# Performance work log

Hardware: AMD Instinct MI355X
Metric: run time of the kernel (lower is better)

Reference implementation:

```python
import jax, jax.numpy as jnp
import numpy as np
from jax import lax

B, N, D, H, K = 4096, 25, 256, 8, 3  # batch*frames, nodes, d_model, heads, conv kernel


def _layernorm(x, g, b, eps=1e-5):
    mu = jnp.mean(x, axis=-1, keepdims=True)
    var = jnp.var(x, axis=-1, keepdims=True)
    return (x - mu) * lax.rsqrt(var + eps) * g + b


def _conv1d(x_bdn, w):
    # x_bdn: [B, D, N], w: [D_out, D_in, K], padding=K//2 (same as torch Conv1d)
    return lax.conv_general_dilated(x_bdn, w, window_strides=(1,),
                                    padding=[(K // 2, K // 2)],
                                    dimension_numbers=('NCH', 'OIH', 'NCH'))


def setup_inputs() -> dict:
    key = jax.random.key(0)
    ks = jax.random.split(key, 12)
    x = jax.random.normal(ks[0], (B, N, D), dtype=jnp.float32)
    # symmetric adjacency with self-loops (skeleton graph surrogate)
    a = jax.random.bernoulli(ks[1], 0.3, (N, N))
    adj = a | a.T | jnp.eye(N, dtype=bool)
    cs = 1.0 / np.sqrt(D * K)
    wq = jax.random.normal(ks[2], (D, D, K), dtype=jnp.float32) * cs
    wk = jax.random.normal(ks[3], (D, D, K), dtype=jnp.float32) * cs
    wv = jax.random.normal(ks[4], (D, D, K), dtype=jnp.float32) * cs
    gq = jnp.ones((D,), jnp.float32); bq = jnp.zeros((D,), jnp.float32)
    gk = jnp.ones((D,), jnp.float32); bk = jnp.zeros((D,), jnp.float32)
    gv = jnp.ones((D,), jnp.float32); bv = jnp.zeros((D,), jnp.float32)
    rel_table = jax.random.normal(ks[5], (2 * N - 1, H), dtype=jnp.float32) * 0.02
    local_bias = jnp.zeros((H, N, N), jnp.float32)
    wo = jax.random.normal(ks[6], (D, D), dtype=jnp.float32) * (1.0 / np.sqrt(D))
    bo = jnp.zeros((D,), jnp.float32)
    return dict(x=x, adj=adj, wq=wq, wk=wk, wv=wv, gq=gq, bq=bq, gk=gk, bk=bk,
                gv=gv, bv=bv, rel_table=rel_table, local_bias=local_bias, wo=wo, bo=bo)


def reference(x, adj, wq, wk, wv, gq, bq, gk, bk, gv, bv, rel_table, local_bias, wo, bo):
    b, n, d = x.shape
    h = local_bias.shape[0]
    dk = d // h
    xp = x.transpose(0, 2, 1)  # [B, D, N]
    # conv QKV projection over node axis + per-projection LayerNorm + residual
    q = x + _layernorm(_conv1d(xp, wq).transpose(0, 2, 1), gq, bq)
    k = x + _layernorm(_conv1d(xp, wk).transpose(0, 2, 1), gk, bk)
    v = x + _layernorm(_conv1d(xp, wv).transpose(0, 2, 1), gv, bv)
    qh = q.reshape(b, n, h, dk).transpose(0, 2, 1, 3)  # [B, H, N, dk]
    kh = k.reshape(b, n, h, dk).transpose(0, 2, 1, 3)
    vh = v.reshape(b, n, h, dk).transpose(0, 2, 1, 3)
    scores = jnp.einsum('bhnd,bhmd->bhnm', qh, kh) / np.sqrt(dk)
    # relative positional bias over node indices
    coords = jnp.arange(n)
    idx = coords[:, None] - coords[None, :] + n - 1  # [N, N]
    rel = rel_table[idx].transpose(2, 0, 1)  # [H, N, N]
    scores = scores + rel[None] + local_bias[None]
    # adjacency mask (local attention): non-neighbors -> -inf
    scores = jnp.where(adj[None, None], scores, jnp.finfo(scores.dtype).min)
    attn = jax.nn.softmax(scores, axis=-1)
    out = jnp.einsum('bhnm,bhmd->bhnd', attn, vh)  # [B, H, N, dk]
    out = out.transpose(0, 2, 1, 3).reshape(b, n, d)
    return out @ wo.T + bo
```

## Files before the change

kernel.cpp:

```cpp
#include <hip/hip_runtime.h>

#define BB 4096
#define NN 25
#define DD 256
#define HH 8
#define DKH 32
#define MM (BB*NN)

typedef __bf16 bf16;
typedef bf16 bf16x8 __attribute__((ext_vector_type(8)));
typedef bf16 bf16x4 __attribute__((ext_vector_type(4)));
typedef float f32x4 __attribute__((ext_vector_type(4)));
typedef float f32x16 __attribute__((ext_vector_type(16)));
typedef int   i32x4 __attribute__((ext_vector_type(4)));
typedef _Float16 h16;
typedef h16 h16x2 __attribute__((ext_vector_type(2)));
typedef h16 h16x4 __attribute__((ext_vector_type(4)));
typedef h16 h16x8 __attribute__((ext_vector_type(8)));

__device__ __forceinline__ void async_load16(const void* g, void* l) {
  __builtin_amdgcn_global_load_lds(
      (const __attribute__((address_space(1))) unsigned int*)g,
      (__attribute__((address_space(3))) unsigned int*)l, 16, 0, 0);
}

#define SCHED_FENCE() __builtin_amdgcn_sched_barrier(0)
#define BARRIER() do { SCHED_FENCE(); __builtin_amdgcn_s_barrier(); SCHED_FENCE(); } while (0)

__global__ __launch_bounds__(256) void k_prep(
    const float* __restrict__ x, bf16* __restrict__ xpad,
    const float* __restrict__ wq, const float* __restrict__ wk, const float* __restrict__ wv,
    const float* __restrict__ rel, const float* __restrict__ lb, const float* __restrict__ wo,
    const void* __restrict__ adj_raw,
    bf16* __restrict__ Wt, h16* __restrict__ woF, float* __restrict__ mbF2) {
  if (blockIdx.x < 13824) {
    int idx = (blockIdx.x * 256 + threadIdx.x) * 8;
    const int total = BB * 27 * 256;
    if (idx >= total) return;
    int b = idx / (27 * 256);
    int rem = idx - b * 27 * 256;
    int j = rem >> 8;
    int d = rem & 255;
    bf16x8 o;
    if (j >= 1 && j <= 25) {
      const float* src = x + ((b * 25 + (j - 1)) * 256 + d);
      #pragma unroll
      for (int t = 0; t < 8; ++t) o[t] = (bf16)src[t];
    } else {
      #pragma unroll
      for (int t = 0; t < 8; ++t) o[t] = (bf16)0.0f;
    }
    *(bf16x8*)(xpad + idx) = o;
    return;
  }
  const int NWT = 768 * 768;
  const int NMB = HH * 64 * 16;
  const int NWF = 8 * 16 * 64 * 8;
  const int total = NWT + NMB + NWF;
  for (int i = (blockIdx.x - 13824) * 256 + threadIdx.x; i < total; i += 512 * 256) {
    if (i < NWT) {
      int j = i / 768, kk = i - j * 768;
      int proj = j >> 8, jo = j & 255;
      int tap = kk >> 8, di = kk & 255;
      const float* w = (proj == 0) ? wq : ((proj == 1) ? wk : wv);
      Wt[i] = (bf16)w[(jo * 256 + di) * 3 + tap];
    } else if (i < NWT + NMB) {
      int t = i - NWT;
      int h = t >> 10;
      int L = (t >> 4) & 63;
      int r = t & 15;
      int iq = L & 31;
      int m = (r & 3) + 8 * (r >> 2) + 4 * (L >> 5);
      float v;
      if (m >= 25) {
        v = -1e30f;
      } else if (iq >= 25) {
        v = 0.0f;
      } else {
        const unsigned char* bytes = (const unsigned char*)adj_raw;
        bool u8 = false;
        for (int s = 0; s < 625; ++s) {
          if ((s & 3) && bytes[s]) { u8 = true; break; }
        }
        int amask = u8 ? (bytes[iq * 25 + m] ? 1 : 0)
                       : (((const int*)adj_raw)[iq * 25 + m] ? 1 : 0);
        v = amask ? (rel[(iq - m + 24) * HH + h] + lb[h * 625 + iq * 25 + m]) : -1e30f;
      }
      mbF2[t] = v;
    } else {
      int e = i - NWT - NMB;
      int c = e & 7, ln = (e >> 3) & 63, nt = (e >> 9) & 15, ks = e >> 13;
      int col = nt * 16 + (ln & 15);
      int k = ks * 32 + (ln >> 4) * 8 + c;
      woF[e] = (h16)wo[col * 256 + k];
    }
  }
}

__global__ __launch_bounds__(512, 2) void k_qkv_gemm8(const bf16* __restrict__ xpad,
                                                      const bf16* __restrict__ Wt,
                                                      bf16* __restrict__ conv) {
  __shared__ bf16 Ab[2][256 * 64];
  __shared__ bf16 Bb[2][256 * 64];

  const int L = blockIdx.x;
  const int sw = (L & 7) * 150 + (L >> 3);
  const int n0 = (sw % 3) * 256;
  const int m0 = (sw / 3) * 256;

  const int tid = threadIdx.x;
  const int lane = tid & 63, wave = tid >> 6;
  const int t16 = lane & 15, quad = lane >> 4;
  const int wr = wave >> 2, wc = wave & 3;

  const int srow = tid >> 3;
  const int sc = ((tid & 7) << 4) ^ ((srow & 7) << 4);
  int aOff[4], bOff[4];
  #pragma unroll
  for (int q = 0; q < 4; ++q) {
    int row = q * 64 + srow;
    int gm = m0 + row;
    int b = gm / 25;
    int n = gm - b * 25;
    aOff[q] = (b * 27 + n) * 512 + sc;
    bOff[q] = (n0 + row) * 1536 + sc;
  }

  const int axr = (t16 & 7) << 3;
  int aoffs[2], boffs[2];
  #pragma unroll
  for (int kk = 0; kk < 2; ++kk) {
    aoffs[kk] = (wr * 128 + t16) * 64 + ((kk * 32 + quad * 8) ^ axr);
    boffs[kk] = (wc * 64 + t16) * 64 + ((kk * 32 + quad * 8) ^ axr);
  }

  f32x4 acc[8][4];
  #pragma unroll
  for (int i = 0; i < 8; ++i)
    #pragma unroll
    for (int j = 0; j < 4; ++j) acc[i][j] = (f32x4){0.f, 0.f, 0.f, 0.f};

  #define ST_B(bufi, tt) do {                                              \
    char* lb_ = (char*)&Bb[bufi][0] + wave * 1024;                         \
    _Pragma("unroll")                                                      \
    for (int q_ = 0; q_ < 4; ++q_)                                         \
      async_load16((const char*)Wt + bOff[q_] + (tt) * 128, lb_ + q_ * 8192); \
  } while (0)
  #define ST_A(bufi, tt) do {                                              \
    char* la_ = (char*)&Ab[bufi][0] + wave * 1024;                         \
    const int ka_ = ((tt) >> 2) * 512 + ((tt) & 3) * 128;                  \
    _Pragma("unroll")                                                      \
    for (int q_ = 0; q_ < 4; ++q_)                                         \
      async_load16((const char*)xpad + aOff[q_] + ka_, la_ + q_ * 8192);   \
  } while (0)

  ST_B(0, 0); ST_A(0, 0);
  ST_B(1, 1); ST_A(1, 1);
  asm volatile("s_waitcnt vmcnt(8)" ::: "memory");
  SCHED_FENCE();
  BARRIER();

  bf16x8 aLo[8], aHi[8], bLo[4], bHi[4];
  {
    const bf16* Ac = &Ab[0][0];
    const bf16* Bc = &Bb[0][0];
    #pragma unroll
    for (int i = 0; i < 4; ++i)
      #pragma unroll
      for (int kk = 0; kk < 2; ++kk)
        aLo[i * 2 + kk] = *(const bf16x8*)(Ac + aoffs[kk] + i * 1024);
    #pragma unroll
    for (int j = 0; j < 2; ++j)
      #pragma unroll
      for (int kk = 0; kk < 2; ++kk)
        bLo[j * 2 + kk] = *(const bf16x8*)(Bc + boffs[kk] + j * 1024);
  }
  SCHED_FENCE();

  for (int u = 0; u < 12; ++u) {
    const int buf = u & 1;
    const bf16* Ac = &Ab[buf][0];
    const bf16* Bc = &Bb[buf][0];
    const bf16* Ac2 = &Ab[buf ^ 1][0];
    const bf16* Bc2 = &Bb[buf ^ 1][0];
    const int st = u + 2;

    #pragma unroll
    for (int j = 0; j < 2; ++j)
      #pragma unroll
      for (int kk = 0; kk < 2; ++kk)
        bHi[j * 2 + kk] = *(const bf16x8*)(Bc + boffs[kk] + (2 + j) * 1024);
    SCHED_FENCE();
    __builtin_amdgcn_s_setprio(1);
    #pragma unroll
    for (int i = 0; i < 4; ++i)
      #pragma unroll
      for (int j = 0; j < 2; ++j)
        #pragma unroll
        for (int kk = 0; kk < 2; ++kk)
          acc[i][j] = __builtin_amdgcn_mfma_f32_16x16x32_bf16(
              aLo[i * 2 + kk], bLo[j * 2 + kk], acc[i][j], 0, 0, 0);
    __builtin_amdgcn_s_setprio(0);
    SCHED_FENCE();

    #pragma unroll
    for (int i = 0; i < 4; ++i)
      #pragma unroll
      for (int kk = 0; kk < 2; ++kk)
        aHi[i * 2 + kk] = *(const bf16x8*)(Ac + aoffs[kk] + (4 + i) * 1024);
    SCHED_FENCE();
    __builtin_amdgcn_s_setprio(1);
    #pragma unroll
    for (int i = 0; i < 4; ++i)
      #pragma unroll
      for (int j = 0; j < 2; ++j)
        #pragma unroll
        for (int kk = 0; kk < 2; ++kk)
          acc[i][2 + j] = __builtin_amdgcn_mfma_f32_16x16x32_bf16(
              aLo[i * 2 + kk], bHi[j * 2 + kk], acc[i][2 + j], 0, 0, 0);
    __builtin_amdgcn_s_setprio(0);
    SCHED_FENCE();

    BARRIER();
    if (st < 12) ST_B(buf, st);
    SCHED_FENCE();
    __builtin_amdgcn_s_setprio(1);
    #pragma unroll
    for (int i = 0; i < 4; ++i)
      #pragma unroll
      for (int j = 0; j < 2; ++j)
        #pragma unroll
        for (int kk = 0; kk < 2; ++kk)
          acc[4 + i][j] = __builtin_amdgcn_mfma_f32_16x16x32_bf16(
              aHi[i * 2 + kk], bLo[j * 2 + kk], acc[4 + i][j], 0, 0, 0);
    __builtin_amdgcn_s_setprio(0);
    SCHED_FENCE();

    if (u < 11) {
      if (u < 10) {
        asm volatile("s_waitcnt vmcnt(4)" ::: "memory");
      } else {
        asm volatile("s_waitcnt vmcnt(0)" ::: "memory");
      }
      SCHED_FENCE();
      BARRIER();
      if (st < 12) ST_A(buf, st);
      #pragma unroll
      for (int i = 0; i < 4; ++i)
        #pragma unroll
        for (int kk = 0; kk < 2; ++kk)
          aLo[i * 2 + kk] = *(const bf16x8*)(Ac2 + aoffs[kk] + i * 1024);
      #pragma unroll
      for (int j = 0; j < 2; ++j)
        #pragma unroll
        for (int kk = 0; kk < 2; ++kk)
          bLo[j * 2 + kk] = *(const bf16x8*)(Bc2 + boffs[kk] + j * 1024);
      SCHED_FENCE();
    }
    __builtin_amdgcn_s_setprio(1);
    #pragma unroll
    for (int i = 0; i < 4; ++i)
      #pragma unroll
      for (int j = 0; j < 2; ++j)
        #pragma unroll
        for (int kk = 0; kk < 2; ++kk)
          acc[4 + i][2 + j] = __builtin_amdgcn_mfma_f32_16x16x32_bf16(
              aHi[i * 2 + kk], bHi[j * 2 + kk], acc[4 + i][2 + j], 0, 0, 0);
    __builtin_amdgcn_s_setprio(0);
    SCHED_FENCE();
  }
  #undef ST_A
  #undef ST_B

  #pragma unroll
  for (int i = 0; i < 8; ++i)
    #pragma unroll
    for (int j = 0; j < 4; ++j) {
      const int col = n0 + wc * 64 + j * 16 + t16;
      #pragma unroll
      for (int r = 0; r < 4; ++r) {
        const int rowm = m0 + wr * 128 + i * 16 + quad * 4 + r;
        conv[(size_t)rowm * 768 + col] = (bf16)acc[i][j][r];
      }
    }
}

__global__ __launch_bounds__(256, 3) void k_attn_oproj(
    const bf16* __restrict__ conv, const float* __restrict__ x,
    const float* __restrict__ gq, const float* __restrict__ bq,
    const float* __restrict__ gk, const float* __restrict__ bk,
    const float* __restrict__ gv, const float* __restrict__ bv,
    const float* __restrict__ mbF2, const h16* __restrict__ woF,
    const float* __restrict__ bo, float* __restrict__ out) {
  __shared__ bf16 Cs[19456];
  __shared__ h16 AoS[6400];
  const int b = blockIdx.x;
  const int tid = threadIdx.x;
  const int wave = tid >> 6, lane = tid & 63;

  const char* slab = (const char*)(conv + (size_t)b * 19200);
  for (int c = wave; c < 38; c += 4)
    async_load16(slab + c * 1024 + lane * 16, (char*)Cs + c * 1024);
  asm volatile("s_waitcnt vmcnt(0)" ::: "memory");
  __syncthreads();

  for (int rowi = wave; rowi < 75; rowi += 4) {
    int n = rowi / 3;
    int p = rowi - n * 3;
    const int rbyte = n * 1536 + p * 512 + lane * 8;
    bf16x4 cv = *(const bf16x4*)((const char*)Cs + rbyte);
    float v0 = (float)cv[0], v1 = (float)cv[1], v2 = (float)cv[2], v3 = (float)cv[3];
    float s = v0 + v1 + v2 + v3;
    float ss = v0 * v0 + v1 * v1 + v2 * v2 + v3 * v3;
    #pragma unroll
    for (int o = 32; o; o >>= 1) {
      s += __shfl_xor(s, o);
      ss += __shfl_xor(ss, o);
    }
    float mu = s * (1.0f / 256.0f);
    float var = ss * (1.0f / 256.0f) - mu * mu;
    float rs = rsqrtf(var + 1e-5f);
    const float* gsel = (p == 0) ? gq : ((p == 1) ? gk : gv);
    const float* bsel = (p == 0) ? bq : ((p == 1) ? bk : bv);
    const int dbase = lane * 4;
    f32x4 gg = *(const f32x4*)(gsel + dbase);
    f32x4 b2 = *(const f32x4*)(bsel + dbase);
    f32x4 xv = *(const f32x4*)(x + ((size_t)(b * 25 + n)) * 256 + dbase);
    h16x4 o;
    o[0] = (h16)((v0 - mu) * rs * gg[0] + b2[0] + xv[0]);
    o[1] = (h16)((v1 - mu) * rs * gg[1] + b2[1] + xv[1]);
    o[2] = (h16)((v2 - mu) * rs * gg[2] + b2[2] + xv[2]);
    o[3] = (h16)((v3 - mu) * rs * gg[3] + b2[3] + xv[3]);
    const int wbyte = n * 1536 + ((p * 512 + lane * 8) ^ ((n & 7) << 4));
    *(h16x4*)((char*)Cs + wbyte) = o;
  }
  __syncthreads();

  {
    const int hi = lane >> 5;
    const int dl = lane & 31;
    const int rowc = dl > 24 ? 24 : dl;
    const char* base = (const char*)Cs;
    const float scale = 0.17677669529663687f;

    #pragma unroll 1
    for (int hh = 0; hh < 2; ++hh) {
      const int h = wave * 2 + hh;

      h16x8 aK[2], bQ[2];
      #pragma unroll
      for (int ks = 0; ks < 2; ++ks) {
        const int kb = h * 64 + ks * 32 + hi * 16;
        aK[ks] = *(const h16x8*)(base + rowc * 1536 + ((512 + kb) ^ ((rowc & 7) << 4)));
        bQ[ks] = *(const h16x8*)(base + rowc * 1536 + ((kb) ^ ((rowc & 7) << 4)));
      }
      f32x16 sacc = (f32x16)(0.0f);
      sacc = __builtin_amdgcn_mfma_f32_32x32x16_f16(aK[0], bQ[0], sacc, 0, 0, 0);
      sacc = __builtin_amdgcn_mfma_f32_32x32x16_f16(aK[1], bQ[1], sacc, 0, 0, 0);

      const float* bp = mbF2 + ((h * 64 + lane) << 4);
      f32x4 b4[4];
      #pragma unroll
      for (int c = 0; c < 4; ++c) b4[c] = *(const f32x4*)(bp + 4 * c);
      float p[16];
      #pragma unroll
      for (int r = 0; r < 16; ++r) p[r] = sacc[r] * scale + b4[r >> 2][r & 3];

      float mx = p[0];
      #pragma unroll
      for (int r = 1; r < 16; ++r) mx = fmaxf(mx, p[r]);
      mx = fmaxf(mx, __shfl_xor(mx, 32));
      float sum = 0.f;
      #pragma unroll
      for (int r = 0; r < 16; ++r) { p[r] = __expf(p[r] - mx); sum += p[r]; }
      sum += __shfl_xor(sum, 32);
      const float inv = 1.0f / sum;
      #pragma unroll
      for (int r = 0; r < 16; ++r) p[r] *= inv;

      int c8[8], d8[8];
      #pragma unroll
      for (int k2 = 0; k2 < 8; ++k2) {
        h16x2 t;
        t[0] = (h16)p[2 * k2];
        t[1] = (h16)p[2 * k2 + 1];
        c8[k2] = __builtin_bit_cast(int, t);
      }
      #pragma unroll
      for (int k2 = 0; k2 < 8; ++k2) d8[k2] = __shfl_xor(c8[k2], 32);
      i32x4 f0 = hi ? (i32x4){d8[2], d8[3], c8[2], c8[3]}
                    : (i32x4){c8[0], c8[1], d8[0], d8[1]};
      i32x4 f1 = hi ? (i32x4){d8[6], d8[7], c8[6], c8[7]}
                    : (i32x4){c8[4], c8[5], d8[4], d8[5]};
      h16x8 fragP0 = __builtin_bit_cast(h16x8, f0);
      h16x8 fragP1 = __builtin_bit_cast(h16x8, f1);

      h16x8 vb0, vb1;
      #pragma unroll
      for (int c = 0; c < 8; ++c) {
        const int m0v = hi * 8 + c;
        int m1v = 16 + hi * 8 + c;
        if (m1v > 24) m1v = 24;
        const int cb = 1024 + h * 64 + 2 * dl;
        vb0[c] = *(const h16*)(base + m0v * 1536 + (cb ^ ((m0v & 7) << 4)));
        vb1[c] = *(const h16*)(base + m1v * 1536 + (cb ^ ((m1v & 7) << 4)));
      }

      f32x16 oacc = (f32x16)(0.0f);
      oacc = __builtin_amdgcn_mfma_f32_32x32x16_f16(fragP0, vb0, oacc, 0, 0, 0);
      oacc = __builtin_amdgcn_mfma_f32_32x32x16_f16(fragP1, vb1, oacc, 0, 0, 0);

      #pragma unroll
      for (int r = 0; r < 16; ++r) {
        const int io = (r & 3) + 8 * (r >> 2) + 4 * hi;
        if (io < 25) {
          const int wb = io * 512 + ((h * 64 + 2 * dl) ^ ((io & 7) << 4));
          *(h16*)((char*)AoS + wb) = (h16)oacc[r];
        }
      }
    }
  }
  __syncthreads();

  {
    const int t16 = lane & 15, quad = lane >> 4;
    f32x4 oacc[2][4];
    #pragma unroll
    for (int mt = 0; mt < 2; ++mt)
      #pragma unroll
      for (int jj = 0; jj < 4; ++jj) oacc[mt][jj] = (f32x4){0.f, 0.f, 0.f, 0.f};
    const int arow0 = t16;
    const int arow1 = (16 + t16 > 24) ? 24 : 16 + t16;
    #pragma unroll
    for (int ks = 0; ks < 8; ++ks) {
      h16x8 aF0, aF1;
      {
        const int kb = ks * 64 + quad * 16;
        aF0 = *(const h16x8*)((const char*)AoS + arow0 * 512 + (kb ^ ((arow0 & 7) << 4)));
        aF1 = *(const h16x8*)((const char*)AoS + arow1 * 512 + (kb ^ ((arow1 & 7) << 4)));
      }
      #pragma unroll
      for (int jj = 0; jj < 4; ++jj) {
        const h16x8 bF = *(const h16x8*)(woF + ((ks * 16 + wave * 4 + jj) << 9) + lane * 8);
        oacc[0][jj] = __builtin_amdgcn_mfma_f32_16x16x32_f16(aF0, bF, oacc[0][jj], 0, 0, 0);
        oacc[1][jj] = __builtin_amdgcn_mfma_f32_16x16x32_f16(aF1, bF, oacc[1][jj], 0, 0, 0);
      }
    }
    #pragma unroll
    for (int jj = 0; jj < 4; ++jj) {
      const int col = (wave * 4 + jj) * 16 + t16;
      const float bb = bo[col];
      #pragma unroll
      for (int mt = 0; mt < 2; ++mt)
        #pragma unroll
        for (int r = 0; r < 4; ++r) {
          const int row = mt * 16 + quad * 4 + r;
          if (row < 25)
            out[((size_t)b * 25 + row) * 256 + col] = oacc[mt][jj][r] + bb;
        }
    }
  }
}

extern "C" void kernel_launch(void* const* d_in, const int* in_sizes, int n_in,
                              void* d_out, int out_size, void* d_ws, size_t ws_size,
                              hipStream_t stream) {
  (void)in_sizes; (void)n_in; (void)out_size; (void)ws_size;
  const float* x  = (const float*)d_in[0];
  const void*  adj = d_in[1];
  const float* wq = (const float*)d_in[2];
  const float* wk = (const float*)d_in[3];
  const float* wv = (const float*)d_in[4];
  const float* gq = (const float*)d_in[5];
  const float* bq = (const float*)d_in[6];
  const float* gk = (const float*)d_in[7];
  const float* bk = (const float*)d_in[8];
  const float* gv = (const float*)d_in[9];
  const float* bv = (const float*)d_in[10];
  const float* rel = (const float*)d_in[11];
  const float* lb = (const float*)d_in[12];
  const float* wo = (const float*)d_in[13];
  const float* bo = (const float*)d_in[14];
  float* out = (float*)d_out;

  char* ws = (char*)d_ws;
  size_t off = 0;
  auto alloc = [&](size_t bytes) -> void* {
    void* p = ws + off;
    off += (bytes + 255) & ~(size_t)255;
    return p;
  };
  bf16* xpad = (bf16*)alloc((size_t)BB * 27 * 256 * 2);
  bf16* conv = (bf16*)alloc((size_t)MM * 768 * 2);
  bf16* Wt   = (bf16*)alloc((size_t)768 * 768 * 2);
  h16*  woF  = (h16*)alloc((size_t)65536 * 2);
  float* mbF2 = (float*)alloc((size_t)HH * 64 * 16 * 4);

  hipLaunchKernelGGL(k_prep, dim3(14336), dim3(256), 0, stream,
                     x, xpad, wq, wk, wv, rel, lb, wo, adj, Wt, woF, mbF2);
  hipLaunchKernelGGL(k_qkv_gemm8, dim3(1200), dim3(512), 0, stream, xpad, Wt, conv);
  hipLaunchKernelGGL(k_attn_oproj, dim3(4096), dim3(256), 0, stream,
                     conv, x, gq, bq, gk, bk, gv, bv, mbF2, woF, bo, out);
}
```

Before: 526.2 us.

## Reuse conv LDS slab for attention output to raise occupancy, prefetch x

The attention/out-projection kernel drops its separate AoS shared buffer and writes each head's attention output into that head's own Q columns of the conv slab. The XOR swizzle is narrowed to bits 4-5 so it stays inside each head's 64-byte block, which keeps the write race-free. The smaller LDS footprint allows launch bounds of 4 blocks per CU instead of 3. The x residual rows are now prefetched as fp16 while the async slab load is in flight. Separately, the prep kernel's per-thread 625-byte adjacency format scan becomes a wave-wide ballot. Risks are higher VGPR pressure from the 19 prefetched registers and an fp16 residual add that changes rounding slightly.

```diff
diff --git a/kernel.cpp b/kernel.cpp
--- a/kernel.cpp
+++ b/kernel.cpp
@@ -53,6 +53,18 @@
     *(bf16x8*)(xpad + idx) = o;
     return;
   }
+  const unsigned char* abytes = (const unsigned char*)adj_raw;
+  bool anyb = false;
+  {
+    const int ln = threadIdx.x & 63;
+    #pragma unroll
+    for (int t = 0; t < 10; ++t) {
+      int s = ln + t * 64;
+      if (s < 625 && (s & 3) && abytes[s]) anyb = true;
+    }
+  }
+  const bool u8 = __any(anyb);
+
   const int NWT = 768 * 768;
   const int NMB = HH * 64 * 16;
   const int NWF = 8 * 16 * 64 * 8;
@@ -77,12 +89,7 @@
       } else if (iq >= 25) {
         v = 0.0f;
       } else {
-        const unsigned char* bytes = (const unsigned char*)adj_raw;
-        bool u8 = false;
-        for (int s = 0; s < 625; ++s) {
-          if ((s & 3) && bytes[s]) { u8 = true; break; }
-        }
-        int amask = u8 ? (bytes[iq * 25 + m] ? 1 : 0)
+        int amask = u8 ? (abytes[iq * 25 + m] ? 1 : 0)
                        : (((const int*)adj_raw)[iq * 25 + m] ? 1 : 0);
         v = amask ? (rel[(iq - m + 24) * HH + h] + lb[h * 625 + iq * 25 + m]) : -1e30f;
       }
@@ -285,7 +292,7 @@
     }
 }
 
-__global__ __launch_bounds__(256, 3) void k_attn_oproj(
+__global__ __launch_bounds__(256, 4) void k_attn_oproj(
     const bf16* __restrict__ conv, const float* __restrict__ x,
     const float* __restrict__ gq, const float* __restrict__ bq,
     const float* __restrict__ gk, const float* __restrict__ bk,
@@ -293,7 +300,6 @@
     const float* __restrict__ mbF2, const h16* __restrict__ woF,
     const float* __restrict__ bo, float* __restrict__ out) {
   __shared__ bf16 Cs[19456];
-  __shared__ h16 AoS[6400];
   const int b = blockIdx.x;
   const int tid = threadIdx.x;
   const int wave = tid >> 6, lane = tid & 63;
@@ -301,38 +307,58 @@
   const char* slab = (const char*)(conv + (size_t)b * 19200);
   for (int c = wave; c < 38; c += 4)
     async_load16(slab + c * 1024 + lane * 16, (char*)Cs + c * 1024);
+
+  h16x4 xpre[19];
+  #pragma unroll
+  for (int k = 0; k < 19; ++k) {
+    const int rowi = wave + 4 * k;
+    if (rowi < 75) {
+      const int n = rowi / 3;
+      f32x4 xv = *(const f32x4*)(x + ((size_t)(b * 25 + n)) * 256 + lane * 4);
+      h16x4 t;
+      t[0] = (h16)xv[0]; t[1] = (h16)xv[1]; t[2] = (h16)xv[2]; t[3] = (h16)xv[3];
+      xpre[k] = t;
+    } else {
+      xpre[k] = (h16x4){(h16)0.f, (h16)0.f, (h16)0.f, (h16)0.f};
+    }
+  }
+
   asm volatile("s_waitcnt vmcnt(0)" ::: "memory");
   __syncthreads();
 
-  for (int rowi = wave; rowi < 75; rowi += 4) {
-    int n = rowi / 3;
-    int p = rowi - n * 3;
-    const int rbyte = n * 1536 + p * 512 + lane * 8;
-    bf16x4 cv = *(const bf16x4*)((const char*)Cs + rbyte);
-    float v0 = (float)cv[0], v1 = (float)cv[1], v2 = (float)cv[2], v3 = (float)cv[3];
-    float s = v0 + v1 + v2 + v3;
-    float ss = v0 * v0 + v1 * v1 + v2 * v2 + v3 * v3;
-    #pragma unroll
-    for (int o = 32; o; o >>= 1) {
-      s += __shfl_xor(s, o);
-      ss += __shfl_xor(ss, o);
-    }
-    float mu = s * (1.0f / 256.0f);
-    float var = ss * (1.0f / 256.0f) - mu * mu;
-    float rs = rsqrtf(var + 1e-5f);
-    const float* gsel = (p == 0) ? gq : ((p == 1) ? gk : gv);
-    const float* bsel = (p == 0) ? bq : ((p == 1) ? bk : bv);
-    const int dbase = lane * 4;
-    f32x4 gg = *(const f32x4*)(gsel + dbase);
-    f32x4 b2 = *(const f32x4*)(bsel + dbase);
-    f32x4 xv = *(const f32x4*)(x + ((size_t)(b * 25 + n)) * 256 + dbase);
-    h16x4 o;
-    o[0] = (h16)((v0 - mu) * rs * gg[0] + b2[0] + xv[0]);
-    o[1] = (h16)((v1 - mu) * rs * gg[1] + b2[1] + xv[1]);
-    o[2] = (h16)((v2 - mu) * rs * gg[2] + b2[2] + xv[2]);
-    o[3] = (h16)((v3 - mu) * rs * gg[3] + b2[3] + xv[3]);
-    const int wbyte = n * 1536 + ((p * 512 + lane * 8) ^ ((n & 7) << 4));
-    *(h16x4*)((char*)Cs + wbyte) = o;
+  #pragma unroll
+  for (int k = 0; k < 19; ++k) {
+    const int rowi = wave + 4 * k;
+    if (rowi < 75) {
+      const int n = rowi / 3;
+      const int p = rowi - n * 3;
+      const int rbyte = n * 1536 + p * 512 + lane * 8;
+      bf16x4 cv = *(const bf16x4*)((const char*)Cs + rbyte);
+      float v0 = (float)cv[0], v1 = (float)cv[1], v2 = (float)cv[2], v3 = (float)cv[3];
+      float s = v0 + v1 + v2 + v3;
+      float ss = v0 * v0 + v1 * v1 + v2 * v2 + v3 * v3;
+      #pragma unroll
+      for (int o = 32; o; o >>= 1) {
+        s += __shfl_xor(s, o);
+        ss += __shfl_xor(ss, o);
+      }
+      float mu = s * (1.0f / 256.0f);
+      float var = ss * (1.0f / 256.0f) - mu * mu;
+      float rs = rsqrtf(var + 1e-5f);
+      const float* gsel = (p == 0) ? gq : ((p == 1) ? gk : gv);
+      const float* bsel = (p == 0) ? bq : ((p == 1) ? bk : bv);
+      const int dbase = lane * 4;
+      f32x4 gg = *(const f32x4*)(gsel + dbase);
+      f32x4 b2 = *(const f32x4*)(bsel + dbase);
+      h16x4 xh = xpre[k];
+      h16x4 o;
+      o[0] = (h16)((v0 - mu) * rs * gg[0] + b2[0]) + xh[0];
+      o[1] = (h16)((v1 - mu) * rs * gg[1] + b2[1]) + xh[1];
+      o[2] = (h16)((v2 - mu) * rs * gg[2] + b2[2]) + xh[2];
+      o[3] = (h16)((v3 - mu) * rs * gg[3] + b2[3]) + xh[3];
+      const int wbyte = n * 1536 + ((p * 512 + lane * 8) ^ ((n & 3) << 4));
+      *(h16x4*)((char*)Cs + wbyte) = o;
+    }
   }
   __syncthreads();
 
@@ -351,8 +377,8 @@
       #pragma unroll
       for (int ks = 0; ks < 2; ++ks) {
         const int kb = h * 64 + ks * 32 + hi * 16;
-        aK[ks] = *(const h16x8*)(base + rowc * 1536 + ((512 + kb) ^ ((rowc & 7) << 4)));
-        bQ[ks] = *(const h16x8*)(base + rowc * 1536 + ((kb) ^ ((rowc & 7) << 4)));
+        aK[ks] = *(const h16x8*)(base + rowc * 1536 + ((512 + kb) ^ ((rowc & 3) << 4)));
+        bQ[ks] = *(const h16x8*)(base + rowc * 1536 + ((kb) ^ ((rowc & 3) << 4)));
       }
       f32x16 sacc = (f32x16)(0.0f);
       sacc = __builtin_amdgcn_mfma_f32_32x32x16_f16(aK[0], bQ[0], sacc, 0, 0, 0);
@@ -402,8 +428,8 @@
         int m1v = 16 + hi * 8 + c;
         if (m1v > 24) m1v = 24;
         const int cb = 1024 + h * 64 + 2 * dl;
-        vb0[c] = *(const h16*)(base + m0v * 1536 + (cb ^ ((m0v & 7) << 4)));
-        vb1[c] = *(const h16*)(base + m1v * 1536 + (cb ^ ((m1v & 7) << 4)));
+        vb0[c] = *(const h16*)(base + m0v * 1536 + (cb ^ ((m0v & 3) << 4)));
+        vb1[c] = *(const h16*)(base + m1v * 1536 + (cb ^ ((m1v & 3) << 4)));
       }
 
       f32x16 oacc = (f32x16)(0.0f);
@@ -414,8 +440,8 @@
       for (int r = 0; r < 16; ++r) {
         const int io = (r & 3) + 8 * (r >> 2) + 4 * hi;
         if (io < 25) {
-          const int wb = io * 512 + ((h * 64 + 2 * dl) ^ ((io & 7) << 4));
-          *(h16*)((char*)AoS + wb) = (h16)oacc[r];
+          const int wb = io * 1536 + ((h * 64 + 2 * dl) ^ ((io & 3) << 4));
+          *(h16*)((char*)Cs + wb) = (h16)oacc[r];
         }
       }
     }
@@ -436,8 +462,8 @@
       h16x8 aF0, aF1;
       {
         const int kb = ks * 64 + quad * 16;
-        aF0 = *(const h16x8*)((const char*)AoS + arow0 * 512 + (kb ^ ((arow0 & 7) << 4)));
-        aF1 = *(const h16x8*)((const char*)AoS + arow1 * 512 + (kb ^ ((arow1 & 7) << 4)));
+        aF0 = *(const h16x8*)((const char*)Cs + arow0 * 1536 + (kb ^ ((arow0 & 3) << 4)));
+        aF1 = *(const h16x8*)((const char*)Cs + arow1 * 1536 + (kb ^ ((arow1 & 3) << 4)));
       }
       #pragma unroll
       for (int jj = 0; jj < 4; ++jj) {
```

Measured after the change: 459.6 us. -12.7%, faster.
